# Kernel optimization log

Hardware: AMD Instinct MI355X
Metric: run time of the kernel (lower is better)

## Reference

```python
import jax, jax.numpy as jnp
import numpy as np

LN_EPS = 1e-5

def _layernorm_hd(x, gamma, beta):
    # normalize jointly over the last two axes (heads, head_dim), like nn.LayerNorm((h, d))
    mu = jnp.mean(x, axis=(-2, -1), keepdims=True)
    var = jnp.var(x, axis=(-2, -1), keepdims=True)
    return (x - mu) * jax.lax.rsqrt(var + LN_EPS) * gamma + beta

def setup_inputs() -> dict:
    key = jax.random.key(0)
    kU, kX, kq, kk, kv = jax.random.split(key, 5)
    B, N, C, H, D = 4, 8192, 256, 8, 32
    scale = (C ** 2) / H  # hidden_channels**2 / n_heads, as in the torch init
    return {
        "U": jax.random.normal(kU, (B, N, C), dtype=jnp.float32),
        "X": jax.random.uniform(kX, (B, N, 1), dtype=jnp.float32),
        "Wq": jax.random.normal(kq, (1, H, D), dtype=jnp.float32) / scale,
        "Wk": jax.random.normal(kk, (C, H, D), dtype=jnp.float32) / scale,
        "Wv": jax.random.normal(kv, (C, H, D), dtype=jnp.float32) / scale,
        "gamma": jnp.ones((H, D), dtype=jnp.float32),
        "beta": jnp.zeros((H, D), dtype=jnp.float32),
    }

def reference(U, X, Wq, Wk, Wv, gamma, beta):
    # dim_domain = 1 -> einsum command 'bnc,chd->bnhd'
    Xq = jnp.einsum('bnc,chd->bnhd', X, Wq)            # [B,N,H,D]
    Uk = jnp.einsum('bnc,chd->bnhd', U, Wk)
    Uv = jnp.einsum('bnc,chd->bnhd', U, Wv)
    # NOTE: original code applies layernorm_key to BOTH key and value (faithful reproduction)
    Uk = _layernorm_hd(Uk, gamma, beta)
    Uv = _layernorm_hd(Uv, gamma, beta)
    num_points = U.shape[1]
    kv = jnp.einsum('bnhd,bnhe->bhde', Uk, Uv)          # [B,H,D,E] small
    sa = jnp.einsum('bnhd,bhde->bneh', Xq, kv)          # [B,N,E,H]
    return (sa / num_points).reshape(U.shape)
```

## Files before the change

kernel.cpp:

```cpp
#include <hip/hip_runtime.h>
#include <math.h>

#define B_DIM 4
#define N_DIM 8192
#define C_DIM 256
#define LN_EPS 1e-5f
#define WSCALE 4096.0f
#define INV_WSCALE (1.0f/4096.0f)

typedef _Float16 f16x8 __attribute__((ext_vector_type(8)));
typedef _Float16 f16x4 __attribute__((ext_vector_type(4)));
typedef float    f32x4 __attribute__((ext_vector_type(4)));

#define WS_WT    0
#define WS_WG    262144
#define WS_K1    263168
#define WS_K2    263200
#define WS_PART  264192
#define WS_QK    1312768

__global__ void k0_pack_w(const float* __restrict__ Wq,
                          const float* __restrict__ Wk,
                          const float* __restrict__ Wv,
                          const float* __restrict__ gamma,
                          const float* __restrict__ beta,
                          char* __restrict__ ws)
{
    const int t = threadIdx.x;
    if (blockIdx.x < 64) {
        const int gid = blockIdx.x * 256 + t;
        const int l   = gid & 63;
        const int cid = gid >> 6;
        const int nt  = cid >> 3;
        const int kt  = cid & 7;
        const int n   = nt * 16 + (l & 15);
        const int kb  = kt * 32 + ((l >> 4) & 3) * 8;
        const float* __restrict__ Wsrc = (n < 256) ? (Wk + n) : (Wv + (n - 256));
        f16x8 frag;
        #pragma unroll
        for (int j = 0; j < 8; ++j) {
            const float w = Wsrc[(size_t)(kb + j) * C_DIM] * WSCALE;
            frag[j] = (_Float16)w;
        }
        ((f16x8*)(ws + WS_WT))[gid] = frag;
    } else {
        if (t < 256) {
            ((float*)(ws + WS_WG))[t] = Wq[t] * gamma[t];
        }
        if (t < 8) {
            float k1 = 0.f, k2 = 0.f;
            for (int d = 0; d < 32; ++d) {
                const int c = t * 32 + d;
                k1 += Wq[c] * gamma[c];
                k2 += Wq[c] * beta[c];
            }
            ((float*)(ws + WS_K1))[t] = k1;
            ((float*)(ws + WS_K2))[t] = k2;
        }
    }
}

__global__ __launch_bounds__(256, 2)
void k1_mfma_ln_reduce(const float* __restrict__ U,
                       const float* __restrict__ gamma,
                       const float* __restrict__ beta,
                       const char* __restrict__ ws_ro,
                       float* __restrict__ part)
{
    __shared__ char lds[81920];
    float* __restrict__ Cf = (float*)lds;
    char*  __restrict__ Ab = lds + 65536;

    const int t    = threadIdx.x;
    const int lane = t & 63;
    const int w    = t >> 6;
    const int bid  = blockIdx.x;
    const int b    = bid >> 8;
    const int row0 = (bid & 255) * 32;

    {
        const float4* __restrict__ Ug =
            (const float4*)(U + ((size_t)b * N_DIM + row0) * C_DIM);
        float4* __restrict__ S4 = (float4*)lds;
        #pragma unroll
        for (int i = 0; i < 8; ++i) S4[i * 256 + t] = Ug[i * 256 + t];
    }
    __syncthreads();

    {
        const int r  = t >> 3;
        const int cg = t & 7;
        const int swz = (r & 7) << 4;
        const float4* __restrict__ S4 = (const float4*)lds;
        #pragma unroll
        for (int jj = 0; jj < 8; ++jj) {
            const int g = (jj + cg) & 7;
            const float4 v = S4[r * 64 + cg * 8 + g];
            f16x4 h;
            h[0] = (_Float16)v.x; h[1] = (_Float16)v.y;
            h[2] = (_Float16)v.z; h[3] = (_Float16)v.w;
            const int byte = r * 512 + cg * 64 + g * 8;
            *(f16x4*)(Ab + (byte ^ swz)) = h;
        }
    }
    __syncthreads();

    f32x4 acc[2][8];
    #pragma unroll
    for (int m = 0; m < 2; ++m)
        #pragma unroll
        for (int j = 0; j < 8; ++j)
            acc[m][j] = (f32x4)0.0f;

    {
        const f16x8* __restrict__ WT = (const f16x8*)(ws_ro + WS_WT);
        const int l15 = lane & 15;
        const int hi  = (lane >> 4) & 3;
        const int swzA = (l15 & 7) << 4;
        #pragma unroll 2
        for (int kt = 0; kt < 8; ++kt) {
            f16x8 a0 = *(const f16x8*)(Ab + ((0 * 16 + l15) * 512 +
                         ((kt * 64 + hi * 16) ^ swzA)));
            f16x8 a1 = *(const f16x8*)(Ab + ((1 * 16 + l15) * 512 +
                         ((kt * 64 + hi * 16) ^ swzA)));
            #pragma unroll
            for (int j = 0; j < 8; ++j) {
                const f16x8 bfrag = WT[(size_t)(((w * 8 + j) * 8 + kt)) * 64 + lane];
                acc[0][j] = __builtin_amdgcn_mfma_f32_16x16x32_f16(a0, bfrag, acc[0][j], 0, 0, 0);
                acc[1][j] = __builtin_amdgcn_mfma_f32_16x16x32_f16(a1, bfrag, acc[1][j], 0, 0, 0);
            }
        }
    }

    {
        const int l15 = lane & 15;
        const int rg  = (lane >> 4) & 3;
        #pragma unroll
        for (int m = 0; m < 2; ++m)
            #pragma unroll
            for (int j = 0; j < 8; ++j) {
                const int col = (w * 8 + j) * 16 + l15;
                #pragma unroll
                for (int q = 0; q < 4; ++q) {
                    const int row = m * 16 + rg * 4 + q;
                    Cf[row * 512 + (col ^ ((row & 7) << 2))] = acc[m][j][q] * INV_WSCALE;
                }
            }
    }
    __syncthreads();

    float* __restrict__ T_lds = (float*)Ab;
    f32x4* __restrict__ red2  = (f32x4*)(Ab + 1024);
    f32x4* __restrict__ red3  = (f32x4*)(Ab + 1536);
    {
        const int r = t >> 3;
        const int h = t & 7;
        const float4* __restrict__ C4  = (const float4*)lds;
        const float4* __restrict__ WG4 = (const float4*)(ws_ro + WS_WG);
        float sk = 0.f, qkk = 0.f, sv = 0.f, qvv = 0.f, Tacc = 0.f;
        #pragma unroll
        for (int g = 0; g < 8; ++g) {
            const int jg = (g + h) & 7;
            const float4 ck = C4[r * 128 + ((h * 8 + jg) ^ (r & 7))];
            const float4 cv = C4[r * 128 + ((64 + h * 8 + jg) ^ (r & 7))];
            const float4 wg = WG4[h * 8 + jg];
            sk  += ck.x + ck.y + ck.z + ck.w;
            qkk += ck.x*ck.x + ck.y*ck.y + ck.z*ck.z + ck.w*ck.w;
            sv  += cv.x + cv.y + cv.z + cv.w;
            qvv += cv.x*cv.x + cv.y*cv.y + cv.z*cv.z + cv.w*cv.w;
            Tacc += wg.x*ck.x + wg.y*ck.y + wg.z*ck.z + wg.w*ck.w;
        }
        #pragma unroll
        for (int m = 1; m <= 4; m <<= 1) {
            sk  += __shfl_xor(sk,  m, 64);
            qkk += __shfl_xor(qkk, m, 64);
            sv  += __shfl_xor(sv,  m, 64);
            qvv += __shfl_xor(qvv, m, 64);
        }
        T_lds[r * 8 + h] = Tacc;
        if (h == 0) { f32x4 v; v[0]=sk; v[1]=qkk; v[2]=sv; v[3]=qvv; red2[r] = v; }
    }
    __syncthreads();

    if (t < 32) {
        const f32x4 v = red2[t];
        const float muk  = v[0] * (1.f/256.f);
        const float vark = v[1] * (1.f/256.f) - muk * muk;
        const float rsk  = 1.0f / sqrtf(vark + LN_EPS);
        const float muv  = v[2] * (1.f/256.f);
        const float varv = v[3] * (1.f/256.f) - muv * muv;
        const float rsv  = 1.0f / sqrtf(varv + LN_EPS);
        f32x4 o; o[0]=muk; o[1]=rsk; o[2]=muv; o[3]=rsv;
        red3[t] = o;
    }
    __syncthreads();

    {
        const int h  = t >> 5;
        const float K1h = ((const float*)(ws_ro + WS_K1))[h];
        const float K2h = ((const float*)(ws_ro + WS_K2))[h];
        const float gv = gamma[t];
        const float bv = beta[t];
        float qk_acc = 0.f;
        #pragma unroll 4
        for (int r = 0; r < 32; ++r) {
            const f32x4 st = red3[r];
            const float Tv = T_lds[r * 8 + h];
            const float s  = st[1] * (Tv - st[0] * K1h) + K2h;
            const float cvv = Cf[r * 512 + ((256 + t) ^ ((r & 7) << 2))];
            const float lnv = (cvv - st[2]) * st[3] * gv + bv;
            qk_acc = fmaf(s, lnv, qk_acc);
        }
        part[(size_t)bid * 256 + t] = qk_acc;
    }
}

__global__ void k2_reduce(const float* __restrict__ part, float* __restrict__ qk)
{
    __shared__ float red[8][32];
    const int t   = threadIdx.x;
    const int blk = blockIdx.x;
    const int b   = blk >> 3;
    const int cg  = blk & 7;
    const int c   = cg * 32 + (t & 31);
    const int seg = t >> 5;
    float s = 0.f;
    for (int i = seg * 32; i < seg * 32 + 32; ++i)
        s += part[((size_t)b * 256 + i) * 256 + c];
    red[seg][t & 31] = s;
    __syncthreads();
    if (t < 32) {
        float q = 0.f;
        #pragma unroll
        for (int sgi = 0; sgi < 8; ++sgi) q += red[sgi][t];
        qk[b * 256 + cg * 32 + t] = q;
    }
}

__global__ __launch_bounds__(256)
void k3_out(const float* __restrict__ X, const float* __restrict__ qk,
            float* __restrict__ out)
{
    __shared__ float qkp[256];
    const int t = threadIdx.x;
    const int bid = blockIdx.x;
    const int b = bid >> 8;
    const int row0 = (bid & 255) * 32;

    {
        const int h = t & 7;
        const int e = t >> 3;
        qkp[t] = qk[b * 256 + h * 32 + e] * (1.0f / (float)N_DIM);
    }
    __syncthreads();

    const int c4 = (t & 63) * 4;
    const float4 q4 = *(const float4*)&qkp[c4];
    const int rl = t >> 6;

    for (int it = 0; it < 8; ++it) {
        const int row = row0 + it * 4 + rl;
        const float x = X[(size_t)b * N_DIM + row];
        float4 o;
        o.x = x * q4.x; o.y = x * q4.y; o.z = x * q4.z; o.w = x * q4.w;
        *(float4*)&out[((size_t)b * N_DIM + row) * C_DIM + c4] = o;
    }
}

extern "C" void kernel_launch(void* const* d_in, const int* in_sizes, int n_in,
                              void* d_out, int out_size, void* d_ws, size_t ws_size,
                              hipStream_t stream)
{
    const float* U     = (const float*)d_in[0];
    const float* X     = (const float*)d_in[1];
    const float* Wq    = (const float*)d_in[2];
    const float* Wk    = (const float*)d_in[3];
    const float* Wv    = (const float*)d_in[4];
    const float* gamma = (const float*)d_in[5];
    const float* beta  = (const float*)d_in[6];
    float* out = (float*)d_out;

    char* ws = (char*)d_ws;
    float* part = (float*)(ws + WS_PART);
    float* qk   = (float*)(ws + WS_QK);

    k0_pack_w<<<65, 256, 0, stream>>>(Wq, Wk, Wv, gamma, beta, ws);
    k1_mfma_ln_reduce<<<1024, 256, 0, stream>>>(U, gamma, beta, ws, part);
    k2_reduce<<<32, 256, 0, stream>>>(part, qk);
    k3_out<<<1024, 256, 0, stream>>>(X, qk, out);
}
```

Measured before the change: 49.02 us.

## Fold LayerNorm statistics into extra GEMM columns and keep accumulators in registers

Adds extra weight columns holding Wq*gamma products and row sums of Wk/Wv, so the MFMA itself produces the per-row key projection dot and the means. Sum of squares is reduced from register accumulators with shuffles, and the value LayerNorm is folded algebraically into a weighted reduction. This avoids staging the fp32 GEMM output in LDS. Each block now handles 64 rows instead of 32, and U is converted to fp16 while loading straight into LDS. The cost is an extra pack kernel, more registers without the two-blocks-per-CU launch bound, and fp16-scaled sums that may lose precision.

```diff
diff --git a/kernel.cpp b/kernel.cpp
--- a/kernel.cpp
+++ b/kernel.cpp
@@ -7,211 +7,292 @@
 #define LN_EPS 1e-5f
 #define WSCALE 4096.0f
 #define INV_WSCALE (1.0f/4096.0f)
+#define SUM_SCALE 8192.0f
+#define INV_SUM_SCALE (1.0f/8192.0f)
+#define M_SCALE 67108864.0f
+#define INV_M_SCALE (1.0f/67108864.0f)
 
 typedef _Float16 f16x8 __attribute__((ext_vector_type(8)));
-typedef _Float16 f16x4 __attribute__((ext_vector_type(4)));
 typedef float    f32x4 __attribute__((ext_vector_type(4)));
 
 #define WS_WT    0
-#define WS_WG    262144
-#define WS_K1    263168
-#define WS_K2    263200
-#define WS_PART  264192
-#define WS_QK    1312768
-
-__global__ void k0_pack_w(const float* __restrict__ Wq,
-                          const float* __restrict__ Wk,
-                          const float* __restrict__ Wv,
-                          const float* __restrict__ gamma,
-                          const float* __restrict__ beta,
-                          char* __restrict__ ws)
-{
-    const int t = threadIdx.x;
-    if (blockIdx.x < 64) {
-        const int gid = blockIdx.x * 256 + t;
-        const int l   = gid & 63;
-        const int cid = gid >> 6;
-        const int nt  = cid >> 3;
-        const int kt  = cid & 7;
-        const int n   = nt * 16 + (l & 15);
-        const int kb  = kt * 32 + ((l >> 4) & 3) * 8;
-        const float* __restrict__ Wsrc = (n < 256) ? (Wk + n) : (Wv + (n - 256));
+#define WS_EXT   270336
+#define WS_K1    286720
+#define WS_K2    286752
+#define WS_PART  286976
+#define WS_QK    811264
+
+__global__ void k0a_ext(const float* __restrict__ Wq,
+                        const float* __restrict__ Wk,
+                        const float* __restrict__ Wv,
+                        const float* __restrict__ gamma,
+                        const float* __restrict__ beta,
+                        char* __restrict__ ws)
+{
+    const int gid = blockIdx.x * 256 + threadIdx.x;
+    const int k = gid >> 3;
+    const int h = gid & 7;
+
+    const float* __restrict__ wkrow = Wk + (size_t)k * C_DIM;
+    const float* __restrict__ wvrow = Wv + (size_t)k * C_DIM;
+
+    float m = 0.f, pk = 0.f, pv = 0.f;
+    #pragma unroll 8
+    for (int d = 0; d < 32; ++d) {
+        const int c = h * 32 + d;
+        const float wg = Wq[c] * gamma[c];
+        const float a = wkrow[c];
+        const float v = wvrow[c];
+        m  = fmaf(a, wg, m);
+        pk += a;
+        pv += v;
+    }
+    #pragma unroll
+    for (int msk = 1; msk <= 4; msk <<= 1) {
+        pk += __shfl_xor(pk, msk, 64);
+        pv += __shfl_xor(pv, msk, 64);
+    }
+    float* __restrict__ ext = (float*)(ws + WS_EXT);
+    ext[k * 16 + h] = m * M_SCALE;
+    if (h == 0) ext[k * 16 + 8] = pk * SUM_SCALE;
+    if (h == 1) ext[k * 16 + 9] = pv * SUM_SCALE;
+    if (h >= 2) ext[k * 16 + 8 + h] = 0.f;
+
+    if (blockIdx.x == 0 && threadIdx.x < 8) {
+        const int hh = threadIdx.x;
+        float k1v = 0.f, k2v = 0.f;
+        for (int d = 0; d < 32; ++d) {
+            const int c = hh * 32 + d;
+            k1v = fmaf(Wq[c], gamma[c], k1v);
+            k2v = fmaf(Wq[c], beta[c],  k2v);
+        }
+        ((float*)(ws + WS_K1))[hh] = k1v;
+        ((float*)(ws + WS_K2))[hh] = k2v;
+    }
+}
+
+__global__ void k0b_pack(const float* __restrict__ Wk,
+                         const float* __restrict__ Wv,
+                         char* __restrict__ ws)
+{
+    __shared__ float Wl[256 * 16];
+    const int t  = threadIdx.x;
+    const int nt = blockIdx.x;
+    const int ci = t & 15;
+    const int kk = t >> 4;
+
+    const float* __restrict__ ext = (const float*)(ws + WS_EXT);
+    #pragma unroll
+    for (int i = 0; i < 16; ++i) {
+        const int k = i * 16 + kk;
+        float v;
+        if (nt < 16)      v = Wk[(size_t)k * C_DIM + nt * 16 + ci] * WSCALE;
+        else if (nt < 32) v = Wv[(size_t)k * C_DIM + (nt - 16) * 16 + ci] * WSCALE;
+        else              v = ext[k * 16 + ci];
+        Wl[k * 16 + ci] = v;
+    }
+    __syncthreads();
+
+    f16x8* __restrict__ WT = (f16x8*)(ws + WS_WT);
+    const int lane = t & 63;
+    const int l15  = lane & 15;
+    const int hi   = lane >> 4;
+    for (int kt = (t >> 6); kt < 8; kt += 4) {
         f16x8 frag;
         #pragma unroll
-        for (int j = 0; j < 8; ++j) {
-            const float w = Wsrc[(size_t)(kb + j) * C_DIM] * WSCALE;
-            frag[j] = (_Float16)w;
-        }
-        ((f16x8*)(ws + WS_WT))[gid] = frag;
-    } else {
-        if (t < 256) {
-            ((float*)(ws + WS_WG))[t] = Wq[t] * gamma[t];
-        }
-        if (t < 8) {
-            float k1 = 0.f, k2 = 0.f;
-            for (int d = 0; d < 32; ++d) {
-                const int c = t * 32 + d;
-                k1 += Wq[c] * gamma[c];
-                k2 += Wq[c] * beta[c];
-            }
-            ((float*)(ws + WS_K1))[t] = k1;
-            ((float*)(ws + WS_K2))[t] = k2;
-        }
-    }
-}
-
-__global__ __launch_bounds__(256, 2)
+        for (int j = 0; j < 8; ++j)
+            frag[j] = (_Float16)Wl[(kt * 32 + hi * 8 + j) * 16 + l15];
+        WT[(nt * 8 + kt) * 64 + lane] = frag;
+    }
+}
+
+__global__ __launch_bounds__(256)
 void k1_mfma_ln_reduce(const float* __restrict__ U,
                        const float* __restrict__ gamma,
                        const float* __restrict__ beta,
                        const char* __restrict__ ws_ro,
                        float* __restrict__ part)
 {
-    __shared__ char lds[81920];
-    float* __restrict__ Cf = (float*)lds;
-    char*  __restrict__ Ab = lds + 65536;
+    __shared__ char lds[41088];
+    float*  __restrict__ T_lds = (float*)(lds + 32768);
+    float*  __restrict__ skv   = (float*)(lds + 34816);
+    float*  __restrict__ qq    = (float*)(lds + 35328);
+    float*  __restrict__ sraw  = (float*)(lds + 36352);
+    float*  __restrict__ sr    = (float*)(lds + 38400);
+    float2* __restrict__ vv    = (float2*)(lds + 40448);
+    float2* __restrict__ DS1   = (float2*)(lds + 40960);
 
     const int t    = threadIdx.x;
     const int lane = t & 63;
     const int w    = t >> 6;
+    const int l15  = lane & 15;
+    const int rg   = lane >> 4;
     const int bid  = blockIdx.x;
-    const int b    = bid >> 8;
-    const int row0 = (bid & 255) * 32;
+    const int b    = bid >> 7;
+    const int row0 = (bid & 127) * 64;
 
     {
-        const float4* __restrict__ Ug =
-            (const float4*)(U + ((size_t)b * N_DIM + row0) * C_DIM);
-        float4* __restrict__ S4 = (float4*)lds;
-        #pragma unroll
-        for (int i = 0; i < 8; ++i) S4[i * 256 + t] = Ug[i * 256 + t];
-    }
-    __syncthreads();
-
-    {
-        const int r  = t >> 3;
-        const int cg = t & 7;
-        const int swz = (r & 7) << 4;
-        const float4* __restrict__ S4 = (const float4*)lds;
-        #pragma unroll
-        for (int jj = 0; jj < 8; ++jj) {
-            const int g = (jj + cg) & 7;
-            const float4 v = S4[r * 64 + cg * 8 + g];
-            f16x4 h;
-            h[0] = (_Float16)v.x; h[1] = (_Float16)v.y;
-            h[2] = (_Float16)v.z; h[3] = (_Float16)v.w;
-            const int byte = r * 512 + cg * 64 + g * 8;
-            *(f16x4*)(Ab + (byte ^ swz)) = h;
-        }
-    }
-    __syncthreads();
-
-    f32x4 acc[2][8];
+        const float* __restrict__ Ub = U + ((size_t)b * N_DIM + row0) * C_DIM;
+        #pragma unroll
+        for (int i = 0; i < 8; ++i) {
+            const int id = i * 256 + t;
+            const int r  = id >> 5;
+            const int kc = id & 31;
+            const float4* __restrict__ src =
+                (const float4*)(Ub + (size_t)r * C_DIM + kc * 8);
+            const float4 v0 = src[0];
+            const float4 v1 = src[1];
+            f16x8 hv;
+            hv[0] = (_Float16)v0.x; hv[1] = (_Float16)v0.y;
+            hv[2] = (_Float16)v0.z; hv[3] = (_Float16)v0.w;
+            hv[4] = (_Float16)v1.x; hv[5] = (_Float16)v1.y;
+            hv[6] = (_Float16)v1.z; hv[7] = (_Float16)v1.w;
+            const int byte = r * 512 + ((kc * 16) ^ ((r & 7) << 4));
+            *(f16x8*)(lds + byte) = hv;
+        }
+    }
+    __syncthreads();
+
+    f32x4 acc[4][8];
+    f32x4 acce[4];
     #pragma unroll
-    for (int m = 0; m < 2; ++m)
-        #pragma unroll
-        for (int j = 0; j < 8; ++j)
-            acc[m][j] = (f32x4)0.0f;
-
+    for (int m = 0; m < 4; ++m) {
+        #pragma unroll
+        for (int j = 0; j < 8; ++j) acc[m][j] = (f32x4)0.0f;
+        acce[m] = (f32x4)0.0f;
+    }
     {
         const f16x8* __restrict__ WT = (const f16x8*)(ws_ro + WS_WT);
-        const int l15 = lane & 15;
-        const int hi  = (lane >> 4) & 3;
-        const int swzA = (l15 & 7) << 4;
+        const int swz = (l15 & 7) << 4;
         #pragma unroll 2
         for (int kt = 0; kt < 8; ++kt) {
-            f16x8 a0 = *(const f16x8*)(Ab + ((0 * 16 + l15) * 512 +
-                         ((kt * 64 + hi * 16) ^ swzA)));
-            f16x8 a1 = *(const f16x8*)(Ab + ((1 * 16 + l15) * 512 +
-                         ((kt * 64 + hi * 16) ^ swzA)));
+            const int boff = ((kt * 64 + rg * 16) ^ swz) + l15 * 512;
+            const f16x8 a0 = *(const f16x8*)(lds + boff);
+            const f16x8 a1 = *(const f16x8*)(lds + boff + 8192);
+            const f16x8 a2 = *(const f16x8*)(lds + boff + 16384);
+            const f16x8 a3 = *(const f16x8*)(lds + boff + 24576);
             #pragma unroll
             for (int j = 0; j < 8; ++j) {
-                const f16x8 bfrag = WT[(size_t)(((w * 8 + j) * 8 + kt)) * 64 + lane];
-                acc[0][j] = __builtin_amdgcn_mfma_f32_16x16x32_f16(a0, bfrag, acc[0][j], 0, 0, 0);
-                acc[1][j] = __builtin_amdgcn_mfma_f32_16x16x32_f16(a1, bfrag, acc[1][j], 0, 0, 0);
-            }
-        }
+                const f16x8 bf = WT[(size_t)((w * 8 + j) * 8 + kt) * 64 + lane];
+                acc[0][j] = __builtin_amdgcn_mfma_f32_16x16x32_f16(a0, bf, acc[0][j], 0, 0, 0);
+                acc[1][j] = __builtin_amdgcn_mfma_f32_16x16x32_f16(a1, bf, acc[1][j], 0, 0, 0);
+                acc[2][j] = __builtin_amdgcn_mfma_f32_16x16x32_f16(a2, bf, acc[2][j], 0, 0, 0);
+                acc[3][j] = __builtin_amdgcn_mfma_f32_16x16x32_f16(a3, bf, acc[3][j], 0, 0, 0);
+            }
+            if (w == 0) {
+                const f16x8 bf = WT[(size_t)(32 * 8 + kt) * 64 + lane];
+                acce[0] = __builtin_amdgcn_mfma_f32_16x16x32_f16(a0, bf, acce[0], 0, 0, 0);
+                acce[1] = __builtin_amdgcn_mfma_f32_16x16x32_f16(a1, bf, acce[1], 0, 0, 0);
+                acce[2] = __builtin_amdgcn_mfma_f32_16x16x32_f16(a2, bf, acce[2], 0, 0, 0);
+                acce[3] = __builtin_amdgcn_mfma_f32_16x16x32_f16(a3, bf, acce[3], 0, 0, 0);
+            }
+        }
+    }
+
+    if (w == 0) {
+        #pragma unroll
+        for (int m = 0; m < 4; ++m)
+            #pragma unroll
+            for (int q = 0; q < 4; ++q) {
+                const int row = m * 16 + rg * 4 + q;
+                const float val = acce[m][q];
+                if (l15 < 8)       T_lds[row * 8 + l15] = val * INV_M_SCALE;
+                else if (l15 == 8) skv[row * 2 + 0] = val * INV_SUM_SCALE;
+                else if (l15 == 9) skv[row * 2 + 1] = val * INV_SUM_SCALE;
+            }
     }
 
     {
-        const int l15 = lane & 15;
-        const int rg  = (lane >> 4) & 3;
-        #pragma unroll
-        for (int m = 0; m < 2; ++m)
-            #pragma unroll
-            for (int j = 0; j < 8; ++j) {
-                const int col = (w * 8 + j) * 16 + l15;
+        float qp[16];
+        #pragma unroll
+        for (int m = 0; m < 4; ++m)
+            #pragma unroll
+            for (int q = 0; q < 4; ++q) {
+                float s = 0.f;
                 #pragma unroll
-                for (int q = 0; q < 4; ++q) {
-                    const int row = m * 16 + rg * 4 + q;
-                    Cf[row * 512 + (col ^ ((row & 7) << 2))] = acc[m][j][q] * INV_WSCALE;
+                for (int j = 0; j < 8; ++j) {
+                    const float v = acc[m][j][q];
+                    s = fmaf(v, v, s);
                 }
-            }
-    }
-    __syncthreads();
-
-    float* __restrict__ T_lds = (float*)Ab;
-    f32x4* __restrict__ red2  = (f32x4*)(Ab + 1024);
-    f32x4* __restrict__ red3  = (f32x4*)(Ab + 1536);
-    {
-        const int r = t >> 3;
-        const int h = t & 7;
-        const float4* __restrict__ C4  = (const float4*)lds;
-        const float4* __restrict__ WG4 = (const float4*)(ws_ro + WS_WG);
-        float sk = 0.f, qkk = 0.f, sv = 0.f, qvv = 0.f, Tacc = 0.f;
-        #pragma unroll
-        for (int g = 0; g < 8; ++g) {
-            const int jg = (g + h) & 7;
-            const float4 ck = C4[r * 128 + ((h * 8 + jg) ^ (r & 7))];
-            const float4 cv = C4[r * 128 + ((64 + h * 8 + jg) ^ (r & 7))];
-            const float4 wg = WG4[h * 8 + jg];
-            sk  += ck.x + ck.y + ck.z + ck.w;
-            qkk += ck.x*ck.x + ck.y*ck.y + ck.z*ck.z + ck.w*ck.w;
-            sv  += cv.x + cv.y + cv.z + cv.w;
-            qvv += cv.x*cv.x + cv.y*cv.y + cv.z*cv.z + cv.w*cv.w;
-            Tacc += wg.x*ck.x + wg.y*ck.y + wg.z*ck.z + wg.w*ck.w;
-        }
-        #pragma unroll
-        for (int m = 1; m <= 4; m <<= 1) {
-            sk  += __shfl_xor(sk,  m, 64);
-            qkk += __shfl_xor(qkk, m, 64);
-            sv  += __shfl_xor(sv,  m, 64);
-            qvv += __shfl_xor(qvv, m, 64);
-        }
-        T_lds[r * 8 + h] = Tacc;
-        if (h == 0) { f32x4 v; v[0]=sk; v[1]=qkk; v[2]=sv; v[3]=qvv; red2[r] = v; }
-    }
-    __syncthreads();
-
-    if (t < 32) {
-        const f32x4 v = red2[t];
-        const float muk  = v[0] * (1.f/256.f);
-        const float vark = v[1] * (1.f/256.f) - muk * muk;
+                qp[m * 4 + q] = s;
+            }
+        #pragma unroll
+        for (int i = 0; i < 16; ++i) {
+            #pragma unroll
+            for (int msk = 1; msk <= 8; msk <<= 1)
+                qp[i] += __shfl_xor(qp[i], msk, 64);
+        }
+        if (l15 == 0) {
+            #pragma unroll
+            for (int m = 0; m < 4; ++m)
+                #pragma unroll
+                for (int q = 0; q < 4; ++q)
+                    qq[w * 64 + m * 16 + rg * 4 + q] = qp[m * 4 + q];
+        }
+    }
+    __syncthreads();
+
+    if (t < 64) {
+        const int r = t;
+        const float sk = skv[r * 2 + 0];
+        const float sv = skv[r * 2 + 1];
+        const float qkk = (qq[0 * 64 + r] + qq[1 * 64 + r]) * (INV_WSCALE * INV_WSCALE);
+        const float qvv = (qq[2 * 64 + r] + qq[3 * 64 + r]) * (INV_WSCALE * INV_WSCALE);
+        const float muk  = sk * (1.f / 256.f);
+        const float vark = qkk * (1.f / 256.f) - muk * muk;
         const float rsk  = 1.0f / sqrtf(vark + LN_EPS);
-        const float muv  = v[2] * (1.f/256.f);
-        const float varv = v[3] * (1.f/256.f) - muv * muv;
+        const float muv  = sv * (1.f / 256.f);
+        const float varv = qvv * (1.f / 256.f) - muv * muv;
         const float rsv  = 1.0f / sqrtf(varv + LN_EPS);
-        f32x4 o; o[0]=muk; o[1]=rsk; o[2]=muv; o[3]=rsv;
-        red3[t] = o;
-    }
-    __syncthreads();
-
-    {
-        const int h  = t >> 5;
-        const float K1h = ((const float*)(ws_ro + WS_K1))[h];
-        const float K2h = ((const float*)(ws_ro + WS_K2))[h];
-        const float gv = gamma[t];
-        const float bv = beta[t];
-        float qk_acc = 0.f;
+        vv[r] = make_float2(muv, rsv);
+        const float* __restrict__ K1 = (const float*)(ws_ro + WS_K1);
+        const float* __restrict__ K2 = (const float*)(ws_ro + WS_K2);
+        #pragma unroll
+        for (int h = 0; h < 8; ++h) {
+            const float Tv = T_lds[r * 8 + h];
+            const float s  = fmaf(rsk, Tv - muk * K1[h], K2[h]);
+            sraw[h * 64 + r] = s;
+            sr[h * 64 + r]   = s * rsv * INV_WSCALE;
+        }
+    }
+    __syncthreads();
+
+    if (t < 8) {
+        const int h = t;
+        float D = 0.f, S1 = 0.f;
         #pragma unroll 4
-        for (int r = 0; r < 32; ++r) {
-            const f32x4 st = red3[r];
-            const float Tv = T_lds[r * 8 + h];
-            const float s  = st[1] * (Tv - st[0] * K1h) + K2h;
-            const float cvv = Cf[r * 512 + ((256 + t) ^ ((r & 7) << 2))];
-            const float lnv = (cvv - st[2]) * st[3] * gv + bv;
-            qk_acc = fmaf(s, lnv, qk_acc);
-        }
-        part[(size_t)bid * 256 + t] = qk_acc;
+        for (int r = 0; r < 64; ++r) {
+            const float s = sraw[h * 64 + r];
+            const float2 mv = vv[r];
+            D  = fmaf(s, mv.x * mv.y, D);
+            S1 += s;
+        }
+        DS1[h] = make_float2(D, S1);
+    }
+    __syncthreads();
+
+    if (w >= 2) {
+        #pragma unroll
+        for (int j = 0; j < 8; ++j) {
+            const int h = (w - 2) * 4 + (j >> 1);
+            float p = 0.f;
+            #pragma unroll
+            for (int m = 0; m < 4; ++m) {
+                const f32x4 s4 = *(const f32x4*)&sr[h * 64 + m * 16 + rg * 4];
+                p = fmaf(s4[0], acc[m][j][0], p);
+                p = fmaf(s4[1], acc[m][j][1], p);
+                p = fmaf(s4[2], acc[m][j][2], p);
+                p = fmaf(s4[3], acc[m][j][3], p);
+            }
+            p += __shfl_xor(p, 16, 64);
+            p += __shfl_xor(p, 32, 64);
+            if (rg == 0) {
+                const int c = (w - 2) * 128 + j * 16 + l15;
+                const float2 ds = DS1[h];
+                part[(size_t)bid * 256 + c] =
+                    fmaf(gamma[c], p - ds.x, beta[c] * ds.y);
+            }
+        }
     }
 }
 
@@ -225,8 +306,8 @@
     const int c   = cg * 32 + (t & 31);
     const int seg = t >> 5;
     float s = 0.f;
-    for (int i = seg * 32; i < seg * 32 + 32; ++i)
-        s += part[((size_t)b * 256 + i) * 256 + c];
+    for (int i = seg * 16; i < seg * 16 + 16; ++i)
+        s += part[((size_t)b * 128 + i) * 256 + c];
     red[seg][t & 31] = s;
     __syncthreads();
     if (t < 32) {
@@ -284,8 +365,9 @@
     float* part = (float*)(ws + WS_PART);
     float* qk   = (float*)(ws + WS_QK);
 
-    k0_pack_w<<<65, 256, 0, stream>>>(Wq, Wk, Wv, gamma, beta, ws);
-    k1_mfma_ln_reduce<<<1024, 256, 0, stream>>>(U, gamma, beta, ws, part);
+    k0a_ext<<<8, 256, 0, stream>>>(Wq, Wk, Wv, gamma, beta, ws);
+    k0b_pack<<<33, 256, 0, stream>>>(Wk, Wv, ws);
+    k1_mfma_ln_reduce<<<512, 256, 0, stream>>>(U, gamma, beta, ws, part);
     k2_reduce<<<32, 256, 0, stream>>>(part, qk);
     k3_out<<<1024, 256, 0, stream>>>(X, qk, out);
 }
```

New measurement: 68.79 us. 40.3% more time.
